# Kernel tuning notes

Measured on AMD Instinct MI355X. Metric: run time of the kernel, lower is better.

The kernel has to match this reference:

```python
import jax, jax.numpy as jnp
import numpy as np

HDIM = 1024
CDIM = 256
TEMPER = 10.0
IGNORE_OUT = 0.0
EPS = 1e-6


def setup_inputs() -> dict:
    key = jax.random.key(0)
    ks = jax.random.split(key, 6)
    B, T, D = 2, 128, 384
    x = jax.random.normal(ks[0], (B, T, D), jnp.float32)
    y = jax.random.normal(ks[1], (B, T, D), jnp.float32)
    # xavier-normal style init for the two linear layers
    W_enc = jax.random.normal(ks[2], (D, HDIM), jnp.float32) * np.sqrt(2.0 / (D + HDIM))
    b_enc = jnp.zeros((HDIM,), jnp.float32)
    W_dec = jax.random.normal(ks[3], (HDIM, D), jnp.float32) * np.sqrt(2.0 / (D + HDIM))
    b_dec = jnp.zeros((D,), jnp.float32)
    return {"x": x, "y": y, "W_enc": W_enc, "b_enc": b_enc, "W_dec": W_dec, "b_dec": b_dec}


def reference(x, y, W_enc, b_enc, W_dec, b_dec):
    B, T, D = x.shape
    n_iter = HDIM // CDIM
    pad = D - 1
    # shift_idx[s, j] = s + j : window of width D at offset s, s in [0, 2D-2]
    shift_idx = jnp.arange(2 * D - 1)[:, None] + jnp.arange(D)[None, :]

    seq_mask = (y == IGNORE_OUT)                       # (B,T,D) bool
    denom_seq = jnp.sum(~seq_mask).astype(x.dtype)
    qn = jnp.linalg.norm(y, axis=-1)                   # (B,T)

    mask_prev = None
    x_dis, losses = [], []
    for _ in range(n_iter):
        # --- _pad_for_shift: (B,T,2D-1,D) shifted windows of x ---
        kp = jnp.pad(x, ((0, 0), (0, 0), (pad, pad)))  # (B,T,3D-2)
        kpt = kp[..., shift_idx]                       # (B,T,2D-1,D)
        # --- _score (cos) + argmax over shifts ---
        kn = jnp.linalg.norm(kpt, axis=-1)             # (B,T,2D-1)
        sim = jnp.einsum('btsd,btd->bts', kpt, y) / (qn[..., None] * kn + EPS)
        sim = jnp.where(jnp.isnan(sim), 0.0, sim)
        theta = jnp.argmax(sim, axis=-1)               # (B,T) int
        x_opt = jnp.take_along_axis(kpt, theta[..., None, None], axis=-2)[..., 0, :]  # (B,T,D)
        # --- attention: elementwise cos-scaled score, temp softmax, detached ---
        dn = (jnp.linalg.norm(x_opt, axis=-1, keepdims=True)
              * jnp.linalg.norm(y, axis=-1, keepdims=True) + EPS)
        attn = jax.nn.softmax((x_opt * y / dn) / TEMPER, axis=-1)
        attn = jnp.where(jnp.isnan(attn), 0.0, attn)
        attn = jax.lax.stop_gradient(attn)
        x_attn = x_opt * attn
        # --- _reverse_pad_for_shift: window at offset 2D-2-theta ---
        kp2 = jnp.pad(x_attn, ((0, 0), (0, 0), (pad, pad)))
        rev_idx = (2 * D - 2 - theta)[..., None] + jnp.arange(D)  # (B,T,D)
        x_ele = jnp.take_along_axis(kp2, rev_idx, axis=-1)         # (B,T,D)
        # --- self_net: encoder -> top-k sparsify -> decoder_self ---
        h = x_ele @ W_enc + b_enc                      # (B,T,HDIM)
        if mask_prev is not None:
            h = jnp.where(mask_prev > 0, 1e-10, h)
        _, idx_top = jax.lax.top_k(h, CDIM)            # (B,T,CDIM)
        flat = idx_top.reshape(B * T, CDIM)
        mask_cur = jnp.zeros((B * T, HDIM), x.dtype).at[
            jnp.arange(B * T)[:, None], flat].set(1.0).reshape(B, T, HDIM)
        if mask_prev is None:
            mask_prev = mask_cur
        else:
            mask_prev = mask_prev + mask_cur - mask_prev * mask_cur
        h = h * mask_cur
        out = h @ W_dec + b_dec                        # (B,T,D)
        x_dis.append(out)
        # --- SeqLoss (masked MSE, mean-reduced by count of valid elems) ---
        err = jnp.where(seq_mask, 0.0, (out - x) ** 2) / denom_seq
        losses.append(jnp.sum(err))
    return jnp.stack(x_dis), jnp.stack(losses)
```

## Files before the change

### kernel.cpp

```cpp
#include <hip/hip_runtime.h>
#include <math.h>

#define DD 384
#define HD 1024
#define CD 256
#define NS 765
#define NITER 4
#define NROWS 256
#define TEMPER_F 10.0f
#define EPSF 1e-6f
#define CUTF 1e-10f

typedef unsigned long long u64;
typedef unsigned int u32;

__device__ __forceinline__ u32 flipf(float f) {
    u32 u = __float_as_uint(f);
    return u ^ ((u32)((int)u >> 31) | 0x80000000u);
}
__device__ __forceinline__ float unflipf(u32 s) {
    u32 fl = ~s;
    u32 u = (fl & 0x80000000u) ? (fl ^ 0x80000000u) : ~fl;
    return __uint_as_float(u);
}
__device__ __forceinline__ u64 shflx64(u64 v, int m) {
    int lo = __shfl_xor((int)(u32)v, m, 64);
    int hi = __shfl_xor((int)(u32)(v >> 32), m, 64);
    return ((u64)(u32)hi << 32) | (u32)lo;
}

__global__ __launch_bounds__(512) void fused_kernel(
    const float* __restrict__ x, const float* __restrict__ y,
    const float* __restrict__ Wenc, const float* __restrict__ benc,
    const float* __restrict__ Wdec, const float* __restrict__ bdec,
    float* __restrict__ out_xdis, float* __restrict__ lossp,
    int* __restrict__ ycnt)
{
    const int row  = blockIdx.x;
    const int tid  = threadIdx.x;
    const int lane = tid & 63;
    const int wid  = tid >> 6;

    __shared__ __align__(16) float xpad[1152];
    __shared__ __align__(16) float yr[DD];
    __shared__ float xa[DD];
    __shared__ __align__(16) float xe_s[DD];
    __shared__ __align__(16) float hpart[HD];
    __shared__ __align__(16) u64   skey[HD];
    __shared__ __align__(16) uint2 dec2[HD];
    __shared__ float wred[8];
    __shared__ int   wredi[8];
    __shared__ float wredn[8];
    __shared__ float s_sc[4];
    __shared__ int   s_theta, s_fb;
    __shared__ float loss4[NITER];

    const float* xrow = x + row * DD;
    const float* yrow = y + row * DD;

    for (int i = tid; i < 1152; i += 512)
        xpad[i] = (i >= DD - 1 && i < 2 * DD - 1) ? xrow[i - (DD - 1)] : 0.f;
    if (tid < DD) yr[tid] = yrow[tid];
    __syncthreads();

    if (tid < DD) {
        float p = yr[tid] * yr[tid];
        int   c = (yr[tid] != 0.f) ? 1 : 0;
        for (int o = 32; o; o >>= 1) {
            p += __shfl_xor(p, o, 64);
            c += __shfl_xor(c, o, 64);
        }
        if (lane == 0) { wred[wid] = p; wredi[wid] = c; }
    }
    __syncthreads();
    if (tid == 0) {
        float s = 0.f; int c = 0;
        for (int w = 0; w < 6; ++w) { s += wred[w]; c += wredi[w]; }
        s_sc[0] = sqrtf(s);
        ycnt[row] = c;
    }
    __syncthreads();
    const float qn = s_sc[0];

    float bv = -INFINITY; int bs = 0x7fffffff; float bn = 0.f;
    if (tid < 192) {
        const float4* xp4 = (const float4*)xpad;
        const float4* yp4 = (const float4*)yr;
        float4 A = xp4[tid];
        const float f0 = A.x * A.x, f1 = A.y * A.y, f2 = A.z * A.z;
        float d0 = 0.f, d1 = 0.f, d2 = 0.f, d3 = 0.f, n0 = 0.f;
#pragma unroll 4
        for (int jc = 0; jc < 96; ++jc) {
            float4 B = xp4[tid + jc + 1];
            float4 Y = yp4[jc];
            d0 += A.x * Y.x; d0 += A.y * Y.y; d0 += A.z * Y.z; d0 += A.w * Y.w;
            d1 += A.y * Y.x; d1 += A.z * Y.y; d1 += A.w * Y.z; d1 += B.x * Y.w;
            d2 += A.z * Y.x; d2 += A.w * Y.y; d2 += B.x * Y.z; d2 += B.y * Y.w;
            d3 += A.w * Y.x; d3 += B.x * Y.y; d3 += B.y * Y.z; d3 += B.z * Y.w;
            n0 += A.x * A.x; n0 += A.y * A.y; n0 += A.z * A.z; n0 += A.w * A.w;
            A = B;
        }
        const float n1 = n0 - f0 + A.x * A.x;
        const float n2 = n1 - f1 + A.y * A.y;
        const float n3 = n2 - f2 + A.z * A.z;
        const int s0 = 4 * tid;
        float sim0 = d0 / (qn * sqrtf(n0) + EPSF);
        float sim1 = d1 / (qn * sqrtf(n1) + EPSF);
        float sim2 = d2 / (qn * sqrtf(n2) + EPSF);
        float sim3 = d3 / (qn * sqrtf(n3) + EPSF);
        bv = sim0; bs = s0; bn = n0;
        if (s0 + 1 < NS && sim1 > bv) { bv = sim1; bs = s0 + 1; bn = n1; }
        if (s0 + 2 < NS && sim2 > bv) { bv = sim2; bs = s0 + 2; bn = n2; }
        if (s0 + 3 < NS && sim3 > bv) { bv = sim3; bs = s0 + 3; bn = n3; }
    }
    for (int o = 32; o; o >>= 1) {
        float v2 = __shfl_xor(bv, o, 64);
        int   i2 = __shfl_xor(bs, o, 64);
        float n2 = __shfl_xor(bn, o, 64);
        if (v2 > bv || (v2 == bv && i2 < bs)) { bv = v2; bs = i2; bn = n2; }
    }
    if (lane == 0) { wred[wid] = bv; wredi[wid] = bs; wredn[wid] = bn; }
    __syncthreads();
    if (tid == 0) {
        float v = wred[0]; int b = wredi[0]; float nn = wredn[0];
        for (int w = 1; w < 8; ++w)
            if (wred[w] > v || (wred[w] == v && wredi[w] < b)) {
                v = wred[w]; b = wredi[w]; nn = wredn[w];
            }
        s_theta = b;
        s_sc[1] = sqrtf(nn) * qn + EPSF;
    }
    __syncthreads();
    const int theta = s_theta;
    const float dn = s_sc[1];

    float xo = 0.f, z = 0.f;
    if (tid < DD) {
        xo = xpad[theta + tid];
        z = (xo * yr[tid] / dn) / TEMPER_F;
        float m = z;
        for (int o = 32; o; o >>= 1) { float w2 = __shfl_xor(m, o, 64); if (w2 > m) m = w2; }
        if (lane == 0) wred[wid] = m;
    }
    __syncthreads();
    if (tid == 0) {
        float m = wred[0];
        for (int w = 1; w < 6; ++w) if (wred[w] > m) m = wred[w];
        s_sc[2] = m;
    }
    __syncthreads();
    float ez = 0.f;
    if (tid < DD) {
        ez = expf(z - s_sc[2]);
        float p = ez;
        for (int o = 32; o; o >>= 1) p += __shfl_xor(p, o, 64);
        if (lane == 0) wred[wid] = p;
    }
    __syncthreads();
    if (tid == 0) {
        float s = 0.f;
        for (int w = 0; w < 6; ++w) s += wred[w];
        s_sc[3] = s;
    }
    __syncthreads();
    if (tid < DD) xa[tid] = xo * (ez / s_sc[3]);
    __syncthreads();
    if (tid < DD) {
        int sj = tid - (theta - (DD - 1));
        xe_s[tid] = (sj >= 0 && sj < DD) ? xa[sj] : 0.f;
    }
    __syncthreads();

    const int c4 = tid & 255;
    const int jh = tid >> 8;
    float4 acc = make_float4(0.f, 0.f, 0.f, 0.f);
    {
        const float* wbase = Wenc + (size_t)(jh * 192) * HD + 4 * c4;
        const float* xb = xe_s + jh * 192;
#pragma unroll 8
        for (int j = 0; j < 192; ++j) {
            float xv = xb[j];
            float4 w = *(const float4*)(wbase + (size_t)j * HD);
            acc.x += xv * w.x; acc.y += xv * w.y;
            acc.z += xv * w.z; acc.w += xv * w.w;
        }
    }
    if (jh == 1) *(float4*)&hpart[4 * c4] = acc;
    if (tid == 0) s_fb = HD;
    if (tid < NITER) loss4[tid] = 0.f;
    __syncthreads();
    if (jh == 0) {
        float4 hp = *(const float4*)&hpart[4 * c4];
        float4 bb = *(const float4*)&benc[4 * c4];
        hp.x += acc.x + bb.x;
        hp.y += acc.y + bb.y;
        hp.z += acc.z + bb.z;
        hp.w += acc.w + bb.w;
        *(float4*)&hpart[4 * c4] = hp;
    }
    __syncthreads();

    float2 hh = *(const float2*)&hpart[2 * tid];
    u64 e0 = ((u64)(~flipf(hh.x)) << 32) | (u32)(2 * tid);
    u64 e1 = ((u64)(~flipf(hh.y)) << 32) | (u32)(2 * tid + 1);

    for (int k = 2; k <= HD; k <<= 1) {
        const bool up = ((2 * tid) & k) == 0;
        for (int j = k >> 1; j > 0; j >>= 1) {
            if (j == 1) {
                bool sw = up ? (e0 > e1) : (e0 < e1);
                if (sw) { u64 t2 = e0; e0 = e1; e1 = t2; }
            } else if (j <= 64) {
                const int m = j >> 1;
                u64 p0 = shflx64(e0, m);
                u64 p1 = shflx64(e1, m);
                const bool takeMin = (((tid & m) == 0) == up);
                e0 = takeMin ? (e0 < p0 ? e0 : p0) : (e0 > p0 ? e0 : p0);
                e1 = takeMin ? (e1 < p1 ? e1 : p1) : (e1 > p1 ? e1 : p1);
            } else {
                __syncthreads();
                skey[2 * tid]     = e0;
                skey[2 * tid + 1] = e1;
                __syncthreads();
                const int tp = tid ^ (j >> 1);
                u64 p0 = skey[2 * tp];
                u64 p1 = skey[2 * tp + 1];
                const bool takeMin = (((tid & (j >> 1)) == 0) == up);
                e0 = takeMin ? (e0 < p0 ? e0 : p0) : (e0 > p0 ? e0 : p0);
                e1 = takeMin ? (e1 < p1 ? e1 : p1) : (e1 > p1 ? e1 : p1);
            }
        }
    }

    {
        float v0 = unflipf((u32)(e0 >> 32));
        float v1 = unflipf((u32)(e1 >> 32));
        dec2[2 * tid]     = make_uint2(__float_as_uint(v0), ((u32)e0) * DD);
        dec2[2 * tid + 1] = make_uint2(__float_as_uint(v1), ((u32)e1) * DD);
        int fbloc = HD;
        if (!(v1 > CUTF)) fbloc = 2 * tid + 1;
        if (!(v0 > CUTF)) fbloc = 2 * tid;
        for (int o = 32; o; o >>= 1) { int t2 = __shfl_xor(fbloc, o, 64); if (t2 < fbloc) fbloc = t2; }
        if (lane == 0) atomicMin(&s_fb, fbloc);
    }
    __syncthreads();
    const int fb = s_fb;

    {
        const int k = tid >> 7;
        const int g = tid & 127;
        const bool active = (g < 96);
        int n = 0;
        if (active) {
            n = (k == 0) ? CD : fb - k * CD;
            if (n < 0) n = 0; if (n > CD) n = CD;
        }
        float4 oacc = make_float4(0.f, 0.f, 0.f, 0.f);
        if (active) oacc = *(const float4*)&bdec[4 * g];
        const float* wd = Wdec + 4 * g;
        const int base = k * CD;
        int r = 0;
        for (; r + 8 <= n; r += 8) {
#pragma unroll
            for (int q = 0; q < 8; q += 2) {
                uint4 dv = *(const uint4*)&dec2[base + r + q];
                float v0 = __uint_as_float(dv.x);
                float4 w0 = *(const float4*)(wd + dv.y);
                float v1 = __uint_as_float(dv.z);
                float4 w1 = *(const float4*)(wd + dv.w);
                oacc.x += v0 * w0.x; oacc.y += v0 * w0.y;
                oacc.z += v0 * w0.z; oacc.w += v0 * w0.w;
                oacc.x += v1 * w1.x; oacc.y += v1 * w1.y;
                oacc.z += v1 * w1.z; oacc.w += v1 * w1.w;
            }
        }
        for (; r < n; ++r) {
            uint2 dv = dec2[base + r];
            float v0 = __uint_as_float(dv.x);
            float4 w0 = *(const float4*)(wd + dv.y);
            oacc.x += v0 * w0.x; oacc.y += v0 * w0.y;
            oacc.z += v0 * w0.z; oacc.w += v0 * w0.w;
        }
        float l = 0.f;
        if (active) {
            *(float4*)&out_xdis[((size_t)k * NROWS + row) * DD + 4 * g] = oacc;
            float4 xv = *(const float4*)&xrow[4 * g];
            float4 yv = *(const float4*)&yr[4 * g];
            float e;
            e = oacc.x - xv.x; if (yv.x != 0.f) l += e * e;
            e = oacc.y - xv.y; if (yv.y != 0.f) l += e * e;
            e = oacc.z - xv.z; if (yv.z != 0.f) l += e * e;
            e = oacc.w - xv.w; if (yv.w != 0.f) l += e * e;
        }
        for (int o = 32; o; o >>= 1) l += __shfl_xor(l, o, 64);
        if (lane == 0) atomicAdd(&loss4[k], l);
    }
    __syncthreads();
    if (tid < NITER) lossp[row * NITER + tid] = loss4[tid];
}

__global__ __launch_bounds__(256) void finalize2(
    const float* __restrict__ lossp, const int* __restrict__ ycnt,
    float* __restrict__ losses)
{
    const int tid = threadIdx.x, lane = tid & 63, w = tid >> 6;
    __shared__ int ctot[4];
    int c = ycnt[tid];
    for (int o = 32; o; o >>= 1) c += __shfl_xor(c, o, 64);
    if (lane == 0) ctot[w] = c;
    __syncthreads();
    const int total = ctot[0] + ctot[1] + ctot[2] + ctot[3];
    float s = lossp[lane * NITER + w] + lossp[(lane + 64) * NITER + w]
            + lossp[(lane + 128) * NITER + w] + lossp[(lane + 192) * NITER + w];
    for (int o = 32; o; o >>= 1) s += __shfl_xor(s, o, 64);
    if (lane == 0) losses[w] = s / (float)total;
}

extern "C" void kernel_launch(void* const* d_in, const int* in_sizes, int n_in,
                              void* d_out, int out_size, void* d_ws, size_t ws_size,
                              hipStream_t stream) {
    const float* x    = (const float*)d_in[0];
    const float* y    = (const float*)d_in[1];
    const float* Wenc = (const float*)d_in[2];
    const float* benc = (const float*)d_in[3];
    const float* Wdec = (const float*)d_in[4];
    const float* bdec = (const float*)d_in[5];

    float* out  = (float*)d_out;
    float* loss = out + (out_size - NITER);

    float* lossp = (float*)d_ws;
    int*   ycnt  = (int*)(lossp + NROWS * NITER);

    fused_kernel<<<NROWS, 512, 0, stream>>>(x, y, Wenc, benc, Wdec, bdec,
                                            out, lossp, ycnt);
    finalize2<<<1, 256, 0, stream>>>(lossp, ycnt, loss);
}
```

Baseline: 113.1 us.

## Split fused kernel into prep, tiled encoder GEMM, and sort/decode kernels

The single per-row kernel is split into three. A prep kernel computes the shifted attention input, a tiled GEMM computes the encoder projection for 8 rows per block, and a third kernel does the top-k sort and sparse decode. The aim is to reuse each W_enc tile across several rows instead of streaming the full weight matrix once per row. In exchange it adds kernel launches and global-memory round trips for the intermediate activations.

```diff
diff --git a/kernel.cpp b/kernel.cpp
--- a/kernel.cpp
+++ b/kernel.cpp
@@ -29,12 +29,9 @@
     return ((u64)(u32)hi << 32) | (u32)lo;
 }
 
-__global__ __launch_bounds__(512) void fused_kernel(
+__global__ __launch_bounds__(384) void prep_kernel(
     const float* __restrict__ x, const float* __restrict__ y,
-    const float* __restrict__ Wenc, const float* __restrict__ benc,
-    const float* __restrict__ Wdec, const float* __restrict__ bdec,
-    float* __restrict__ out_xdis, float* __restrict__ lossp,
-    int* __restrict__ ycnt)
+    float* __restrict__ xe_g, int* __restrict__ ycnt)
 {
     const int row  = blockIdx.x;
     const int tid  = threadIdx.x;
@@ -44,26 +41,21 @@
     __shared__ __align__(16) float xpad[1152];
     __shared__ __align__(16) float yr[DD];
     __shared__ float xa[DD];
-    __shared__ __align__(16) float xe_s[DD];
-    __shared__ __align__(16) float hpart[HD];
-    __shared__ __align__(16) u64   skey[HD];
-    __shared__ __align__(16) uint2 dec2[HD];
     __shared__ float wred[8];
     __shared__ int   wredi[8];
     __shared__ float wredn[8];
     __shared__ float s_sc[4];
-    __shared__ int   s_theta, s_fb;
-    __shared__ float loss4[NITER];
+    __shared__ int   s_theta;
 
     const float* xrow = x + row * DD;
     const float* yrow = y + row * DD;
 
-    for (int i = tid; i < 1152; i += 512)
+    for (int i = tid; i < 1152; i += 384)
         xpad[i] = (i >= DD - 1 && i < 2 * DD - 1) ? xrow[i - (DD - 1)] : 0.f;
-    if (tid < DD) yr[tid] = yrow[tid];
-    __syncthreads();
-
-    if (tid < DD) {
+    yr[tid] = yrow[tid];
+    __syncthreads();
+
+    {
         float p = yr[tid] * yr[tid];
         int   c = (yr[tid] != 0.f) ? 1 : 0;
         for (int o = 32; o; o >>= 1) {
@@ -123,7 +115,7 @@
     __syncthreads();
     if (tid == 0) {
         float v = wred[0]; int b = wredi[0]; float nn = wredn[0];
-        for (int w = 1; w < 8; ++w)
+        for (int w = 1; w < 6; ++w)
             if (wred[w] > v || (wred[w] == v && wredi[w] < b)) {
                 v = wred[w]; b = wredi[w]; nn = wredn[w];
             }
@@ -134,10 +126,9 @@
     const int theta = s_theta;
     const float dn = s_sc[1];
 
-    float xo = 0.f, z = 0.f;
-    if (tid < DD) {
-        xo = xpad[theta + tid];
-        z = (xo * yr[tid] / dn) / TEMPER_F;
+    const float xo = xpad[theta + tid];
+    const float z = (xo * yr[tid] / dn) / TEMPER_F;
+    {
         float m = z;
         for (int o = 32; o; o >>= 1) { float w2 = __shfl_xor(m, o, 64); if (w2 > m) m = w2; }
         if (lane == 0) wred[wid] = m;
@@ -149,9 +140,8 @@
         s_sc[2] = m;
     }
     __syncthreads();
-    float ez = 0.f;
-    if (tid < DD) {
-        ez = expf(z - s_sc[2]);
+    const float ez = expf(z - s_sc[2]);
+    {
         float p = ez;
         for (int o = 32; o; o >>= 1) p += __shfl_xor(p, o, 64);
         if (lane == 0) wred[wid] = p;
@@ -163,46 +153,82 @@
         s_sc[3] = s;
     }
     __syncthreads();
-    if (tid < DD) xa[tid] = xo * (ez / s_sc[3]);
-    __syncthreads();
-    if (tid < DD) {
+    xa[tid] = xo * (ez / s_sc[3]);
+    __syncthreads();
+    {
         int sj = tid - (theta - (DD - 1));
-        xe_s[tid] = (sj >= 0 && sj < DD) ? xa[sj] : 0.f;
-    }
-    __syncthreads();
-
-    const int c4 = tid & 255;
-    const int jh = tid >> 8;
+        xe_g[row * DD + tid] = (sj >= 0 && sj < DD) ? xa[sj] : 0.f;
+    }
+}
+
+__global__ __launch_bounds__(256) void enc_gemm(
+    const float* __restrict__ xe_g, const float* __restrict__ Wenc,
+    const float* __restrict__ benc, float* __restrict__ h_g)
+{
+    const int rt = blockIdx.x >> 5;
+    const int ct = blockIdx.x & 31;
+    const int tid = threadIdx.x;
+    __shared__ float A[8][388];
+    __shared__ __align__(16) float4 part[3][64];
+
+    {
+        const float4* src = (const float4*)(xe_g + (size_t)rt * 8 * DD);
+        for (int i = tid; i < 768; i += 256) {
+            float4 v = src[i];
+            int r = i / 96, c = (i - r * 96) * 4;
+            A[r][c] = v.x; A[r][c+1] = v.y; A[r][c+2] = v.z; A[r][c+3] = v.w;
+        }
+    }
+    __syncthreads();
+
+    const int cq = tid & 7;
+    const int r  = (tid >> 3) & 7;
+    const int ks = tid >> 6;
+    const int col = ct * 32 + cq * 4;
+    const float* wp = Wenc + (size_t)(ks * 96) * HD + col;
+    const float* ar = &A[r][ks * 96];
     float4 acc = make_float4(0.f, 0.f, 0.f, 0.f);
-    {
-        const float* wbase = Wenc + (size_t)(jh * 192) * HD + 4 * c4;
-        const float* xb = xe_s + jh * 192;
 #pragma unroll 8
-        for (int j = 0; j < 192; ++j) {
-            float xv = xb[j];
-            float4 w = *(const float4*)(wbase + (size_t)j * HD);
-            acc.x += xv * w.x; acc.y += xv * w.y;
-            acc.z += xv * w.z; acc.w += xv * w.w;
-        }
-    }
-    if (jh == 1) *(float4*)&hpart[4 * c4] = acc;
+    for (int j = 0; j < 96; ++j) {
+        float a = ar[j];
+        float4 w = *(const float4*)(wp + (size_t)j * HD);
+        acc.x += a * w.x; acc.y += a * w.y;
+        acc.z += a * w.z; acc.w += a * w.w;
+    }
+    if (ks) part[ks - 1][tid & 63] = acc;
+    __syncthreads();
+    if (ks == 0) {
+        float4 p1 = part[0][tid], p2 = part[1][tid], p3 = part[2][tid];
+        float4 bb = *(const float4*)(benc + col);
+        acc.x += p1.x + p2.x + p3.x + bb.x;
+        acc.y += p1.y + p2.y + p3.y + bb.y;
+        acc.z += p1.z + p2.z + p3.z + bb.z;
+        acc.w += p1.w + p2.w + p3.w + bb.w;
+        *(float4*)(h_g + (size_t)(rt * 8 + r) * HD + col) = acc;
+    }
+}
+
+__global__ __launch_bounds__(512) void sortdec_kernel(
+    const float* __restrict__ h_g,
+    const float* __restrict__ Wdec, const float* __restrict__ bdec,
+    const float* __restrict__ x, const float* __restrict__ y,
+    float* __restrict__ out_xdis, float* __restrict__ lossp)
+{
+    const int row  = blockIdx.x;
+    const int tid  = threadIdx.x;
+    const int lane = tid & 63;
+
+    __shared__ __align__(16) u64   skey[HD];
+    __shared__ __align__(16) uint2 dec2[HD];
+    __shared__ int   s_fb;
+    __shared__ float loss4[NITER];
+
+    float2 hh = *(const float2*)(h_g + (size_t)row * HD + 2 * tid);
+    u64 e0 = ((u64)(~flipf(hh.x)) << 32) | (u32)(2 * tid);
+    u64 e1 = ((u64)(~flipf(hh.y)) << 32) | (u32)(2 * tid + 1);
     if (tid == 0) s_fb = HD;
     if (tid < NITER) loss4[tid] = 0.f;
     __syncthreads();
-    if (jh == 0) {
-        float4 hp = *(const float4*)&hpart[4 * c4];
-        float4 bb = *(const float4*)&benc[4 * c4];
-        hp.x += acc.x + bb.x;
-        hp.y += acc.y + bb.y;
-        hp.z += acc.z + bb.z;
-        hp.w += acc.w + bb.w;
-        *(float4*)&hpart[4 * c4] = hp;
-    }
-    __syncthreads();
-
-    float2 hh = *(const float2*)&hpart[2 * tid];
-    u64 e0 = ((u64)(~flipf(hh.x)) << 32) | (u32)(2 * tid);
-    u64 e1 = ((u64)(~flipf(hh.y)) << 32) | (u32)(2 * tid + 1);
 
     for (int k = 2; k <= HD; k <<= 1) {
         const bool up = ((2 * tid) & k) == 0;
@@ -284,8 +310,8 @@
         float l = 0.f;
         if (active) {
             *(float4*)&out_xdis[((size_t)k * NROWS + row) * DD + 4 * g] = oacc;
-            float4 xv = *(const float4*)&xrow[4 * g];
-            float4 yv = *(const float4*)&yr[4 * g];
+            float4 xv = *(const float4*)&x[row * DD + 4 * g];
+            float4 yv = *(const float4*)&y[row * DD + 4 * g];
             float e;
             e = oacc.x - xv.x; if (yv.x != 0.f) l += e * e;
             e = oacc.y - xv.y; if (yv.y != 0.f) l += e * e;
@@ -329,10 +355,13 @@
     float* out  = (float*)d_out;
     float* loss = out + (out_size - NITER);
 
-    float* lossp = (float*)d_ws;
-    int*   ycnt  = (int*)(lossp + NROWS * NITER);
-
-    fused_kernel<<<NROWS, 512, 0, stream>>>(x, y, Wenc, benc, Wdec, bdec,
-                                            out, lossp, ycnt);
+    int*   ycnt  = (int*)d_ws;
+    float* lossp = (float*)(ycnt + NROWS);
+    float* xe_g  = lossp + NROWS * NITER;
+    float* h_g   = xe_g + (size_t)NROWS * DD;
+
+    prep_kernel<<<NROWS, 384, 0, stream>>>(x, y, xe_g, ycnt);
+    enc_gemm<<<1024, 256, 0, stream>>>(xe_g, Wenc, benc, h_g);
+    sortdec_kernel<<<NROWS, 512, 0, stream>>>(h_g, Wdec, bdec, x, y, out, lossp);
     finalize2<<<1, 256, 0, stream>>>(lossp, ycnt, loss);
 }
```

Measured after the change: 115.1 us. About the same (+1.8%).
